# Kernel tuning notes

Hardware: AMD Instinct MI355X
Metric: run time of the kernel (lower is better)

Reference implementation:

```python
import jax, jax.numpy as jnp
import numpy as np

D_MODEL = 1024
NUM_HEADS = 16
D_K = D_MODEL // NUM_HEADS
B, S = 2, 2048
LN_EPS = 1e-5


def setup_inputs() -> dict:
    key = jax.random.key(0)
    ks = jax.random.split(key, 11)
    sc = 1.0 / np.sqrt(D_MODEL)
    return {
        "x": jax.random.normal(ks[0], (B, S, D_MODEL), dtype=jnp.float32),
        "Wq": jax.random.normal(ks[1], (D_MODEL, D_MODEL), dtype=jnp.float32) * sc,
        "bq": jnp.zeros((D_MODEL,), dtype=jnp.float32),
        "Wk": jax.random.normal(ks[2], (D_MODEL, D_MODEL), dtype=jnp.float32) * sc,
        "bk": jnp.zeros((D_MODEL,), dtype=jnp.float32),
        "Wv": jax.random.normal(ks[3], (D_MODEL, D_MODEL), dtype=jnp.float32) * sc,
        "bv": jnp.zeros((D_MODEL,), dtype=jnp.float32),
        "Wo": jax.random.normal(ks[4], (D_MODEL, D_MODEL), dtype=jnp.float32) * sc,
        "bo": jnp.zeros((D_MODEL,), dtype=jnp.float32),
        "ln_gamma": jnp.ones((D_MODEL,), dtype=jnp.float32),
        "ln_beta": jnp.zeros((D_MODEL,), dtype=jnp.float32),
    }


def reference(x, Wq, bq, Wk, bk, Wv, bv, Wo, bo, ln_gamma, ln_beta):
    b, s, d = x.shape
    # QKV projections -> [B, H, S, D_K]
    def split_heads(y):
        return y.reshape(b, s, NUM_HEADS, D_K).transpose(0, 2, 1, 3)
    q = split_heads(x @ Wq + bq)
    k = split_heads(x @ Wk + bk)
    v = split_heads(x @ Wv + bv)
    # scores [B, H, S, S]; dropout is identity in eval mode
    scores = jnp.einsum("bhqd,bhkd->bhqk", q, k) / jnp.sqrt(jnp.float32(D_K))
    attn = jax.nn.softmax(scores, axis=-1)
    context = jnp.einsum("bhqk,bhkd->bhqd", attn, v)
    context = context.transpose(0, 2, 1, 3).reshape(b, s, d)
    out = context @ Wo + bo
    # residual + LayerNorm (eps=1e-5, torch default)
    h = x + out
    mu = jnp.mean(h, axis=-1, keepdims=True)
    var = jnp.var(h, axis=-1, keepdims=True)
    return (h - mu) / jnp.sqrt(var + LN_EPS) * ln_gamma + ln_beta
```

## Files before the change

kernel.cpp:

```cpp
#include <hip/hip_runtime.h>
#include <math.h>

#define D_MODEL 1024
#define NHEAD   16
#define DKK     64
#define BATCH   2
#define SEQ     2048
#define MROWS   (BATCH*SEQ)

typedef __attribute__((ext_vector_type(8)))  short bf16x8;
typedef __attribute__((ext_vector_type(4)))  short bf16x4;
typedef __attribute__((ext_vector_type(4)))  float f32x4;
typedef __attribute__((ext_vector_type(16))) float f32x16;

#define MFMA(a,b,c)   __builtin_amdgcn_mfma_f32_16x16x32_bf16((a),(b),(c),0,0,0)
#define MFMA32(a,b,c) __builtin_amdgcn_mfma_f32_32x32x16_bf16((a),(b),(c),0,0,0)

#define QSCALE 0.18033688f

#define SBAR() { __builtin_amdgcn_sched_barrier(0); \
                 __builtin_amdgcn_s_barrier();      \
                 __builtin_amdgcn_sched_barrier(0); }

#define CH  520
#define TIL (8*CH)

__device__ __forceinline__ short f2b(float f) {
    unsigned u = __float_as_uint(f);
    unsigned r = (u + 0x7FFFu + ((u >> 16) & 1u)) >> 16;
    return (short)r;
}
__device__ __forceinline__ float b2f(short s) {
    return __uint_as_float(((unsigned)(unsigned short)s) << 16);
}

__device__ __forceinline__ float fexp2(float x) {
    float r; asm("v_exp_f32 %0, %1" : "=v"(r) : "v"(x)); return r;
}

__device__ __forceinline__ void gld_lds16(const void* g, void* l) {
    __builtin_amdgcn_global_load_lds(
        (const __attribute__((address_space(1))) void*)g,
        (__attribute__((address_space(3))) void*)l, 16, 0, 0);
}

__global__ __launch_bounds__(256)
void prep_weights(const float* __restrict__ Wq, const float* __restrict__ Wk,
                  const float* __restrict__ Wv, const float* __restrict__ Wo,
                  short* __restrict__ wt3, short* __restrict__ wot)
{
    const int z = blockIdx.z;
    const float* W = z==0 ? Wq : z==1 ? Wk : z==2 ? Wv : Wo;
    short* dst = (z < 3) ? (wt3 + (size_t)z*1024*1024) : wot;
    __shared__ float tile[32][33];
    const int tx = threadIdx.x & 31, ty = threadIdx.x >> 5;
    const int c0 = blockIdx.x*32, r0 = blockIdx.y*32;
    #pragma unroll
    for (int i = 0; i < 4; i++)
        tile[ty + i*8][tx] = W[(size_t)(r0 + ty + i*8)*1024 + c0 + tx];
    __syncthreads();
    #pragma unroll
    for (int i = 0; i < 4; i++)
        dst[(size_t)(c0 + ty + i*8)*1024 + r0 + tx] = f2b(tile[tx][ty + i*8]);
}

__global__ __launch_bounds__(256)
void convert_x(const float* __restrict__ x, short* __restrict__ xb)
{
    const int i = (blockIdx.x*256 + threadIdx.x) * 8;
    float4 a = *(const float4*)(x + i);
    float4 c = *(const float4*)(x + i + 4);
    bf16x8 v;
    v[0]=f2b(a.x); v[1]=f2b(a.y); v[2]=f2b(a.z); v[3]=f2b(a.w);
    v[4]=f2b(c.x); v[5]=f2b(c.y); v[6]=f2b(c.z); v[7]=f2b(c.w);
    *(bf16x8*)(xb + i) = v;
}

__global__ __launch_bounds__(512, 2)
void gemm_qkv(const short* __restrict__ A, const short* __restrict__ Bt,
              const float* __restrict__ bq, const float* __restrict__ bk,
              const float* __restrict__ bv,
              short* __restrict__ qb, short* __restrict__ kb, short* __restrict__ vtb)
{
    __shared__ short Ab[2*16384];
    __shared__ short Bb[2*12288];

    const int t = threadIdx.x;
    const int w = t >> 6, lane = t & 63;
    const int r = lane & 15, g4 = lane >> 4;
    const int wm = w >> 2, wn = w & 3;

    const int bid = blockIdx.x;
    const int xcd = bid & 7, idx = bid >> 3;
    const int mi  = (xcd >> 1) * 4 + (idx & 3);
    const int ni  = (xcd & 1) * 8 + (idx >> 2);
    const int m0 = mi * 256, n0 = ni * 192;

    const int srow = t >> 3;
    const int scol = ((t & 7) ^ (srow & 7)) * 8;

    f32x4 acc[8][3] = {};
    bf16x8 bfr[2][3];

#define QKV_STAGE(P, KT)                                                      \
    { const int kk = (KT) * 64 + scol;                                        \
      _Pragma("unroll")                                                       \
      for (int a = 0; a < 4; a++)                                             \
          gld_lds16(A + (size_t)(m0 + a*64 + srow)*1024 + kk,                 \
                    Ab + (P)*16384 + a*4096 + t*8);                           \
      _Pragma("unroll")                                                       \
      for (int p2 = 0; p2 < 3; p2++)                                          \
          gld_lds16(Bt + (size_t)(n0 + p2*64 + srow)*1024 + kk,               \
                    Bb + (P)*12288 + p2*4096 + t*8); }

#define QKV_PHASE(P, MH, KS, LOADB)                                           \
    { const short* Abase = Ab + (P)*16384 + wm*8192;                          \
      bf16x8 af[4];                                                           \
      _Pragma("unroll")                                                       \
      for (int i = 0; i < 4; i++)                                             \
          af[i] = *(const bf16x8*)&Abase[((MH)*64 + i*16 + r)*64 +            \
                                         (((KS)*4 + g4) ^ (r&7))*8];          \
      if (LOADB) {                                                            \
          const short* Bbase = Bb + (P)*12288;                                \
          _Pragma("unroll")                                                   \
          for (int j = 0; j < 3; j++)                                         \
              bfr[KS][j] = *(const bf16x8*)&Bbase[(wn*48 + j*16 + r)*64 +     \
                                                  (((KS)*4 + g4) ^ (r&7))*8]; \
      }                                                                       \
      SBAR();                                                                 \
      __builtin_amdgcn_s_setprio(1);                                          \
      _Pragma("unroll")                                                       \
      for (int i = 0; i < 4; i++)                                             \
          _Pragma("unroll")                                                   \
          for (int j = 0; j < 3; j++)                                         \
              acc[(MH)*4+i][j] = MFMA(af[i], bfr[KS][j], acc[(MH)*4+i][j]);   \
      __builtin_amdgcn_s_setprio(0);                                          \
      SBAR(); }

    QKV_STAGE(0, 0)
    QKV_STAGE(1, 1)
    asm volatile("s_waitcnt vmcnt(7)" ::: "memory");
    __builtin_amdgcn_s_barrier();
    __builtin_amdgcn_sched_barrier(0);

    int p = 0;
    #pragma unroll 1
    for (int kt = 0; kt < 16; kt++) {
        QKV_PHASE(p, 0, 0, 1)
        QKV_PHASE(p, 1, 0, 0)
        QKV_PHASE(p, 0, 1, 1)
        QKV_PHASE(p, 1, 1, 0)
        if (kt < 14) {
            QKV_STAGE(p, kt + 2)
            asm volatile("s_waitcnt vmcnt(7)" ::: "memory");
        } else {
            asm volatile("s_waitcnt vmcnt(0)" ::: "memory");
        }
        __builtin_amdgcn_s_barrier();
        __builtin_amdgcn_sched_barrier(0);
        p ^= 1;
    }
#undef QKV_STAGE
#undef QKV_PHASE

    #pragma unroll
    for (int n = 0; n < 3; n++) {
        const int colbase = n0 + wn*48 + n*16;
        const int proj    = colbase >> 10;
        const int within  = colbase & 1023;
        const int h       = within >> 6;
        const int d       = (within & 63) + r;
        const float* bias = (proj == 0) ? bq : (proj == 1) ? bk : bv;
        const float bval  = bias[within + r];
        #pragma unroll
        for (int m = 0; m < 8; m++) {
            const int growb = m0 + wm*128 + m*16 + g4*4;
            const int bidx  = growb >> 11;
            const int s     = growb & 2047;
            if (proj == 0) {
                #pragma unroll
                for (int i = 0; i < 4; i++)
                    qb[((size_t)(bidx*NHEAD + h)*SEQ + s + i)*DKK + d] =
                        f2b((acc[m][n][i] + bval) * QSCALE);
            } else if (proj == 1) {
                #pragma unroll
                for (int i = 0; i < 4; i++)
                    kb[((size_t)(bidx*NHEAD + h)*SEQ + s + i)*DKK + d] =
                        f2b(acc[m][n][i] + bval);
            } else {
                bf16x4 pk;
                #pragma unroll
                for (int i = 0; i < 4; i++) pk[i] = f2b(acc[m][n][i] + bval);
                *(bf16x4*)(vtb + ((size_t)(bidx*NHEAD + h)*DKK + d)*SEQ + s) = pk;
            }
        }
    }
}

__global__ __launch_bounds__(256)
void gemm_out(const short* __restrict__ A, const short* __restrict__ Bt,
              const float* __restrict__ bo, const short* __restrict__ resid,
              short* __restrict__ hb)
{
    __shared__ short As[2*128*32];
    __shared__ short Bs[2*64*32];
    const int t = threadIdx.x;
    const int w = t >> 6, lane = t & 63;
    const int r = lane & 15, g4 = lane >> 4;
    const int wr = w >> 1, wc = w & 1;

    const int bid = blockIdx.x;
    const int xcd = bid & 7, idx = bid >> 3;
    const int mi  = (xcd >> 1) * 8 + (idx & 7);
    const int ni  = (xcd & 1) * 8 + (idx >> 3);
    const int m0 = mi * 128, n0 = ni * 64;

    const int srow = lane >> 2, su = lane & 3;

    f32x4 acc[4][2] = {};

#define OUT_STAGE(BUF, K0)                                                     \
    { const int kk = (K0) & 1023;                                              \
      _Pragma("unroll")                                                        \
      for (int c = 0; c < 2; c++) {                                            \
          const int row = w*32 + c*16 + srow;                                  \
          gld_lds16(A + (size_t)(m0+row)*1024 + kk + 8*(su ^ ((row>>1)&3)),    \
                    As + (BUF)*4096 + w*1024 + c*512);                         \
      }                                                                        \
      { const int row = w*16 + srow;                                           \
        gld_lds16(Bt + (size_t)(n0+row)*1024 + kk + 8*(su ^ ((row>>1)&3)),     \
                  Bs + (BUF)*2048 + w*512); } }

    OUT_STAGE(0, 0)
    __syncthreads();

    int cur = 0;
    #pragma unroll 1
    for (int k0 = 0; k0 < 1024; k0 += 32) {
        OUT_STAGE(cur^1, k0 + 32)
        const short* Abase = As + cur*4096;
        const short* Bbase = Bs + cur*2048;
        bf16x8 af[4], bfr[2];
        #pragma unroll
        for (int m = 0; m < 4; m++) {
            const int row = wr*64 + m*16 + r;
            af[m] = *(const bf16x8*)&Abase[row*32 + (g4 ^ ((row>>1)&3))*8];
        }
        #pragma unroll
        for (int n = 0; n < 2; n++) {
            const int row = wc*32 + n*16 + r;
            bfr[n] = *(const bf16x8*)&Bbase[row*32 + (g4 ^ ((row>>1)&3))*8];
        }
        __builtin_amdgcn_s_setprio(1);
        #pragma unroll
        for (int m = 0; m < 4; m++)
            #pragma unroll
            for (int n = 0; n < 2; n++)
                acc[m][n] = MFMA(af[m], bfr[n], acc[m][n]);
        __builtin_amdgcn_s_setprio(0);
        __syncthreads();
        cur ^= 1;
    }
#undef OUT_STAGE

    #pragma unroll
    for (int n = 0; n < 2; n++) {
        const int col = n0 + wc*32 + n*16 + r;
        const float bval = bo[col];
        #pragma unroll
        for (int m = 0; m < 4; m++) {
            #pragma unroll
            for (int i = 0; i < 4; i++) {
                const int grow = m0 + wr*64 + m*16 + g4*4 + i;
                const size_t ofs = (size_t)grow*1024 + col;
                hb[ofs] = f2b(acc[m][n][i] + bval + b2f(resid[ofs]));
            }
        }
    }
}

__global__ __launch_bounds__(256, 2)
void attn_mfma(const short* __restrict__ Q, const short* __restrict__ K,
               const short* __restrict__ VT, short* __restrict__ ctx)
{
    __shared__ short Ks[4*TIL];
    __shared__ short Vs[4*TIL];

    const int t = threadIdx.x;
    const int w = t >> 6, lane = t & 63;
    const int l31 = lane & 31, hi = lane >> 5;
    const int srow8 = lane >> 3, su = lane & 7;
    const int lane8 = lane * 8;
    const int swz8  = (su ^ srow8) * 8;

    const int bid     = blockIdx.x;
    const int logical = (bid & 7) * 64 + (bid >> 3);
    const int bh_lin  = logical >> 4;
    const int qt      = logical & 15;
    const int b = bh_lin >> 4, h = bh_lin & 15;
    const int q0 = qt * 128 + w * 32;

    const size_t bh = (size_t)b * NHEAD + h;
    const short* Qp = Q  + bh * SEQ * DKK;
    const short* Kp = K  + bh * SEQ * DKK;
    const short* Vp = VT + bh * DKK * SEQ;

    const short* kstage = Kp + (size_t)(w*8 + srow8) * DKK + swz8;
    const short* vstage = Vp + (size_t)(w*8 + srow8) * SEQ + swz8;

    bf16x8 qf[4];
    #pragma unroll
    for (int d0 = 0; d0 < 4; d0++)
        qf[d0] = *(const bf16x8*)(Qp + (size_t)(q0 + l31)*DKK + d0*16 + hi*8);

    int koff[8], voff[8];
    #pragma unroll
    for (int i = 0; i < 8; i++) {
        const int kchunk = (i>>2)*4 + (l31>>3);
        koff[i] = kchunk*CH + (l31&7)*64 + ((((i&3)*2 + hi) ^ (l31&7)) * 8);
        const int vchunk = (i&1)*4 + (l31>>3);
        voff[i] = vchunk*CH + (l31&7)*64 + ((((i>>1)*2 + hi) ^ (l31&7)) * 8);
    }

    f32x16 o0A = {}, o1A = {}, o0B = {}, o1B = {};
    float lrow = 0.f;

#define ATT_STAGE(KDST, VDST, J)                                               \
    { const size_t jj = (size_t)((J) & (SEQ-1));                               \
      const short* ksrc = kstage + jj*DKK;                                     \
      gld_lds16(ksrc,           (KDST) + w*CH + lane8);                        \
      gld_lds16(ksrc + 32*DKK,  (KDST) + (4+w)*CH + lane8);                    \
      const short* vsrc = vstage + jj;                                         \
      gld_lds16(vsrc,           (VDST) + w*CH + lane8);                        \
      gld_lds16(vsrc + 32*SEQ,  (VDST) + (4+w)*CH + lane8); }

#define QK_SUB(KB, S0, S1)                                                     \
    { bf16x8 kf[8];                                                            \
      _Pragma("unroll")                                                        \
      for (int i = 0; i < 8; i++) kf[i] = *(const bf16x8*)&(KB)[koff[i]];      \
      _Pragma("unroll")                                                        \
      for (int d0 = 0; d0 < 4; d0++) S0 = MFMA32(kf[d0],   qf[d0], S0);        \
      _Pragma("unroll")                                                        \
      for (int d0 = 0; d0 < 4; d0++) S1 = MFMA32(kf[4+d0], qf[d0], S1); }

#define PV_SUB(S0, S1, VB, O0, O1)                                             \
    { bf16x8 vf[8];                                                            \
      _Pragma("unroll")                                                        \
      for (int i = 0; i < 8; i++) vf[i] = *(const bf16x8*)&(VB)[voff[i]];      \
      _Pragma("unroll")                                                        \
      for (int ks = 0; ks < 4; ks++) {                                         \
        const int g = (ks & 1) * 8;                                            \
        float e0,e1,e2,e3,e4,e5,e6,e7;                                         \
        if (ks < 2) { e0=S0[g+0];e1=S0[g+1];e2=S0[g+2];e3=S0[g+3];             \
                      e4=S0[g+4];e5=S0[g+5];e6=S0[g+6];e7=S0[g+7]; }           \
        else        { e0=S1[g+0];e1=S1[g+1];e2=S1[g+2];e3=S1[g+3];             \
                      e4=S1[g+4];e5=S1[g+5];e6=S1[g+6];e7=S1[g+7]; }           \
        unsigned u0,u1,u2,u3;                                                  \
        asm("v_cvt_pk_bf16_f32 %0, %1, %2" : "=v"(u0) : "v"(e0), "v"(e1));     \
        asm("v_cvt_pk_bf16_f32 %0, %1, %2" : "=v"(u1) : "v"(e2), "v"(e3));     \
        asm("v_cvt_pk_bf16_f32 %0, %1, %2" : "=v"(u2) : "v"(e4), "v"(e5));     \
        asm("v_cvt_pk_bf16_f32 %0, %1, %2" : "=v"(u3) : "v"(e6), "v"(e7));     \
        auto rA = __builtin_amdgcn_permlane32_swap(u0, u2, false, false);      \
        auto rB = __builtin_amdgcn_permlane32_swap(u1, u3, false, false);      \
        union { unsigned u[4]; bf16x8 v; } pa;                                 \
        pa.u[0] = rA[0]; pa.u[1] = rB[0]; pa.u[2] = rA[1]; pa.u[3] = rB[1];    \
        O0 = MFMA32(pa.v, vf[ks*2+0], O0);                                     \
        O1 = MFMA32(pa.v, vf[ks*2+1], O1);                                     \
      } }

    ATT_STAGE(Ks,       Vs,       0)
    ATT_STAGE(Ks + TIL, Vs + TIL, 64)
    __syncthreads();

    int cur = 0;
    #pragma unroll 1
    for (int j0 = 0; j0 < SEQ; j0 += 128) {
        {
            const int nb = (cur^1)*2*TIL;
            ATT_STAGE(Ks + nb,       Vs + nb,       j0 + 128)
            ATT_STAGE(Ks + nb + TIL, Vs + nb + TIL, j0 + 192)
        }

        const short* KbA = Ks + cur*2*TIL;
        const short* VbA = Vs + cur*2*TIL;
        const short* KbB = KbA + TIL;
        const short* VbB = VbA + TIL;

        f32x16 s0A = {}, s1A = {}, s0B = {}, s1B = {};
        QK_SUB(KbA, s0A, s1A)
        QK_SUB(KbB, s0B, s1B)

        #pragma unroll
        for (int r = 0; r < 16; r++) s0A[r] = fexp2(s0A[r]);
        #pragma unroll
        for (int r = 0; r < 16; r++) s1A[r] = fexp2(s1A[r]);
        #pragma unroll
        for (int r = 0; r < 16; r++) s0B[r] = fexp2(s0B[r]);
        #pragma unroll
        for (int r = 0; r < 16; r++) s1B[r] = fexp2(s1B[r]);

        float ts[16];
        #pragma unroll
        for (int r = 0; r < 16; r++) ts[r] = (s0A[r] + s1A[r]) + (s0B[r] + s1B[r]);
        #pragma unroll
        for (int dd = 8; dd >= 1; dd >>= 1)
            #pragma unroll
            for (int r = 0; r < dd; r++) ts[r] += ts[r + dd];
        lrow += ts[0] + __shfl_xor(ts[0], 32);

        PV_SUB(s0A, s1A, VbA, o0A, o1A)
        PV_SUB(s0B, s1B, VbB, o0B, o1B)

        __syncthreads();
        cur ^= 1;
    }

    const float li = 1.f / lrow;
    const int lb = __float_as_int(li);
    #pragma unroll
    for (int r = 0; r < 16; r++) {
        const int crow = (r&3) + 8*(r>>2) + 4*hi;
        const float lv = __int_as_float(__builtin_amdgcn_ds_bpermute(crow*4, lb));
        const size_t base = ((size_t)b*SEQ + q0 + crow)*D_MODEL + h*DKK + l31;
        ctx[base]      = f2b((o0A[r] + o0B[r]) * lv);
        ctx[base + 32] = f2b((o1A[r] + o1B[r]) * lv);
    }
#undef ATT_STAGE
#undef QK_SUB
#undef PV_SUB
}

__global__ __launch_bounds__(256)
void ln_kernel(const short* __restrict__ hbuf, const float* __restrict__ gamma,
               const float* __restrict__ beta, float* __restrict__ out)
{
    const int row = blockIdx.x;
    const int t = threadIdx.x;
    const short* hp = hbuf + (size_t)row * D_MODEL;
    bf16x4 hv = ((const bf16x4*)hp)[t];
    float v0 = b2f(hv[0]), v1 = b2f(hv[1]), v2 = b2f(hv[2]), v3 = b2f(hv[3]);
    float sum = v0 + v1 + v2 + v3;
    float sq  = v0*v0 + v1*v1 + v2*v2 + v3*v3;
    #pragma unroll
    for (int o = 1; o <= 32; o <<= 1) {
        sum += __shfl_xor(sum, o);
        sq  += __shfl_xor(sq, o);
    }
    __shared__ float s1[4], s2[4];
    if ((t & 63) == 0) { s1[t >> 6] = sum; s2[t >> 6] = sq; }
    __syncthreads();
    sum = s1[0] + s1[1] + s1[2] + s1[3];
    sq  = s2[0] + s2[1] + s2[2] + s2[3];
    const float mean = sum * (1.0f / D_MODEL);
    const float var  = sq * (1.0f / D_MODEL) - mean * mean;
    const float inv  = rsqrtf(var + 1e-5f);
    float4 g  = ((const float4*)gamma)[t];
    float4 be = ((const float4*)beta)[t];
    float4 rr;
    rr.x = (v0 - mean) * inv * g.x + be.x;
    rr.y = (v1 - mean) * inv * g.y + be.y;
    rr.z = (v2 - mean) * inv * g.z + be.z;
    rr.w = (v3 - mean) * inv * g.w + be.w;
    ((float4*)(out + (size_t)row * D_MODEL))[t] = rr;
}

extern "C" void kernel_launch(void* const* d_in, const int* in_sizes, int n_in,
                              void* d_out, int out_size, void* d_ws, size_t ws_size,
                              hipStream_t stream)
{
    const float* x  = (const float*)d_in[0];
    const float* Wq = (const float*)d_in[1];
    const float* bq = (const float*)d_in[2];
    const float* Wk = (const float*)d_in[3];
    const float* bk = (const float*)d_in[4];
    const float* Wv = (const float*)d_in[5];
    const float* bv = (const float*)d_in[6];
    const float* Wo = (const float*)d_in[7];
    const float* bo = (const float*)d_in[8];
    const float* g  = (const float*)d_in[9];
    const float* be = (const float*)d_in[10];

    char* base = (char*)d_ws;
    short* xb   = (short*)base;
    short* wt3  = (short*)(base + (8u<<20));
    short* wot  = (short*)(base + (14u<<20));
    short* qb   = (short*)(base + (16u<<20));
    short* kb   = (short*)(base + (24u<<20));
    short* vtb  = (short*)(base + (32u<<20));
    short* cxb  = (short*)(base + (40u<<20));
    short* hb16 = (short*)(base + (48u<<20));

    prep_weights<<<dim3(32,32,4), 256, 0, stream>>>(Wq, Wk, Wv, Wo, wt3, wot);
    convert_x  <<<2048, 256, 0, stream>>>(x, xb);
    gemm_qkv   <<<256, 512, 0, stream>>>(xb, wt3, bq, bk, bv, qb, kb, vtb);
    attn_mfma  <<<512, 256, 0, stream>>>(qb, kb, vtb, cxb);
    gemm_out   <<<512, 256, 0, stream>>>(cxb, wot, bo, xb, hb16);
    ln_kernel  <<<MROWS, 256, 0, stream>>>(hb16, g, be, (float*)d_out);
}
```

Before: 120.5 us.

## Merge prep kernels, transpose V stores via bpermute, defer softmax row-sum reduction

```diff
diff --git a/kernel.cpp b/kernel.cpp
--- a/kernel.cpp
+++ b/kernel.cpp
@@ -45,35 +45,36 @@
 }
 
 __global__ __launch_bounds__(256)
-void prep_weights(const float* __restrict__ Wq, const float* __restrict__ Wk,
-                  const float* __restrict__ Wv, const float* __restrict__ Wo,
-                  short* __restrict__ wt3, short* __restrict__ wot)
+void prep_all(const float* __restrict__ x,
+              const float* __restrict__ Wq, const float* __restrict__ Wk,
+              const float* __restrict__ Wv, const float* __restrict__ Wo,
+              short* __restrict__ xb, short* __restrict__ wt3,
+              short* __restrict__ wot)
 {
     const int z = blockIdx.z;
-    const float* W = z==0 ? Wq : z==1 ? Wk : z==2 ? Wv : Wo;
-    short* dst = (z < 3) ? (wt3 + (size_t)z*1024*1024) : wot;
-    __shared__ float tile[32][33];
-    const int tx = threadIdx.x & 31, ty = threadIdx.x >> 5;
-    const int c0 = blockIdx.x*32, r0 = blockIdx.y*32;
-    #pragma unroll
-    for (int i = 0; i < 4; i++)
-        tile[ty + i*8][tx] = W[(size_t)(r0 + ty + i*8)*1024 + c0 + tx];
-    __syncthreads();
-    #pragma unroll
-    for (int i = 0; i < 4; i++)
-        dst[(size_t)(c0 + ty + i*8)*1024 + r0 + tx] = f2b(tile[tx][ty + i*8]);
-}
-
-__global__ __launch_bounds__(256)
-void convert_x(const float* __restrict__ x, short* __restrict__ xb)
-{
-    const int i = (blockIdx.x*256 + threadIdx.x) * 8;
-    float4 a = *(const float4*)(x + i);
-    float4 c = *(const float4*)(x + i + 4);
-    bf16x8 v;
-    v[0]=f2b(a.x); v[1]=f2b(a.y); v[2]=f2b(a.z); v[3]=f2b(a.w);
-    v[4]=f2b(c.x); v[5]=f2b(c.y); v[6]=f2b(c.z); v[7]=f2b(c.w);
-    *(bf16x8*)(xb + i) = v;
+    if (z < 4) {
+        const float* W = z==0 ? Wq : z==1 ? Wk : z==2 ? Wv : Wo;
+        short* dst = (z < 3) ? (wt3 + (size_t)z*1024*1024) : wot;
+        __shared__ float tile[32][33];
+        const int tx = threadIdx.x & 31, ty = threadIdx.x >> 5;
+        const int c0 = blockIdx.x*32, r0 = blockIdx.y*32;
+        #pragma unroll
+        for (int i = 0; i < 4; i++)
+            tile[ty + i*8][tx] = W[(size_t)(r0 + ty + i*8)*1024 + c0 + tx];
+        __syncthreads();
+        #pragma unroll
+        for (int i = 0; i < 4; i++)
+            dst[(size_t)(c0 + ty + i*8)*1024 + r0 + tx] = f2b(tile[tx][ty + i*8]);
+    } else {
+        const int blk = (z-4)*1024 + blockIdx.y*32 + blockIdx.x;
+        const int i = (blk*256 + threadIdx.x) * 8;
+        float4 a = *(const float4*)(x + i);
+        float4 c = *(const float4*)(x + i + 4);
+        bf16x8 v;
+        v[0]=f2b(a.x); v[1]=f2b(a.y); v[2]=f2b(a.z); v[3]=f2b(a.w);
+        v[4]=f2b(c.x); v[5]=f2b(c.y); v[6]=f2b(c.z); v[7]=f2b(c.w);
+        *(bf16x8*)(xb + i) = v;
+    }
 }
 
 __global__ __launch_bounds__(512, 2)
@@ -163,6 +164,10 @@
 #undef QKV_STAGE
 #undef QKV_PHASE
 
+    const int src4 = ((((lane & 3) << 4) | (lane >> 2)) << 2);
+    const int dl   = lane >> 2;
+    const int sl   = (lane & 3) * 4;
+
     #pragma unroll
     for (int n = 0; n < 3; n++) {
         const int colbase = n0 + wn*48 + n*16;
@@ -188,10 +193,19 @@
                     kb[((size_t)(bidx*NHEAD + h)*SEQ + s + i)*DKK + d] =
                         f2b(acc[m][n][i] + bval);
             } else {
-                bf16x4 pk;
-                #pragma unroll
-                for (int i = 0; i < 4; i++) pk[i] = f2b(acc[m][n][i] + bval);
-                *(bf16x4*)(vtb + ((size_t)(bidx*NHEAD + h)*DKK + d)*SEQ + s) = pk;
+                const int sbase = m0 + wm*128 + m*16;
+                const int bidx2 = sbase >> 11;
+                const int srw   = sbase & 2047;
+                unsigned lo  = ((unsigned)(unsigned short)f2b(acc[m][n][1]+bval) << 16)
+                             |  (unsigned)(unsigned short)f2b(acc[m][n][0]+bval);
+                unsigned hi2 = ((unsigned)(unsigned short)f2b(acc[m][n][3]+bval) << 16)
+                             |  (unsigned)(unsigned short)f2b(acc[m][n][2]+bval);
+                unsigned t0 = (unsigned)__builtin_amdgcn_ds_bpermute(src4, (int)lo);
+                unsigned t1 = (unsigned)__builtin_amdgcn_ds_bpermute(src4, (int)hi2);
+                union { unsigned u[2]; bf16x4 v; } pk4;
+                pk4.u[0] = t0; pk4.u[1] = t1;
+                *(bf16x4*)(vtb + ((size_t)(bidx2*NHEAD + h)*DKK + (within & 63) + dl)*SEQ
+                               + srw + sl) = pk4.v;
             }
         }
     }
@@ -322,8 +336,7 @@
         voff[i] = vchunk*CH + (l31&7)*64 + ((((i>>1)*2 + hi) ^ (l31&7)) * 8);
     }
 
-    f32x16 o0A = {}, o1A = {}, o0B = {}, o1B = {};
-    float lrow = 0.f;
+    f32x16 o0A = {}, o1A = {}, o0B = {}, o1B = {}, lacc = {};
 
 #define ATT_STAGE(KDST, VDST, J)                                               \
     { const size_t jj = (size_t)((J) & (SEQ-1));                               \
@@ -399,14 +412,9 @@
         #pragma unroll
         for (int r = 0; r < 16; r++) s1B[r] = fexp2(s1B[r]);
 
-        float ts[16];
-        #pragma unroll
-        for (int r = 0; r < 16; r++) ts[r] = (s0A[r] + s1A[r]) + (s0B[r] + s1B[r]);
-        #pragma unroll
-        for (int dd = 8; dd >= 1; dd >>= 1)
-            #pragma unroll
-            for (int r = 0; r < dd; r++) ts[r] += ts[r + dd];
-        lrow += ts[0] + __shfl_xor(ts[0], 32);
+        #pragma unroll
+        for (int r = 0; r < 16; r++)
+            lacc[r] += (s0A[r] + s1A[r]) + (s0B[r] + s1B[r]);
 
         PV_SUB(s0A, s1A, VbA, o0A, o1A)
         PV_SUB(s0B, s1B, VbB, o0B, o1B)
@@ -414,6 +422,15 @@
         __syncthreads();
         cur ^= 1;
     }
+
+    float ts[16];
+    #pragma unroll
+    for (int r = 0; r < 16; r++) ts[r] = lacc[r];
+    #pragma unroll
+    for (int dd = 8; dd >= 1; dd >>= 1)
+        #pragma unroll
+        for (int r = 0; r < dd; r++) ts[r] += ts[r + dd];
+    const float lrow = ts[0] + __shfl_xor(ts[0], 32);
 
     const float li = 1.f / lrow;
     const int lb = __float_as_int(li);
@@ -490,10 +507,9 @@
     short* cxb  = (short*)(base + (40u<<20));
     short* hb16 = (short*)(base + (48u<<20));
 
-    prep_weights<<<dim3(32,32,4), 256, 0, stream>>>(Wq, Wk, Wv, Wo, wt3, wot);
-    convert_x  <<<2048, 256, 0, stream>>>(x, xb);
-    gemm_qkv   <<<256, 512, 0, stream>>>(xb, wt3, bq, bk, bv, qb, kb, vtb);
-    attn_mfma  <<<512, 256, 0, stream>>>(qb, kb, vtb, cxb);
-    gemm_out   <<<512, 256, 0, stream>>>(cxb, wot, bo, xb, hb16);
-    ln_kernel  <<<MROWS, 256, 0, stream>>>(hb16, g, be, (float*)d_out);
-}
+    prep_all  <<<dim3(32,32,6), 256, 0, stream>>>(x, Wq, Wk, Wv, Wo, xb, wt3, wot);
+    gemm_qkv  <<<256, 512, 0, stream>>>(xb, wt3, bq, bk, bv, qb, kb, vtb);
+    attn_mfma <<<512, 256, 0, stream>>>(qb, kb, vtb, cxb);
+    gemm_out  <<<512, 256, 0, stream>>>(cxb, wot, bo, xb, hb16);
+    ln_kernel <<<MROWS, 256, 0, stream>>>(hb16, g, be, (float*)d_out);
+}
```

After: 118.6 us. No clear change (-1.6%).
